# Optimization experiments

Hardware: AMD Instinct MI355X
Metric: run time of the kernel (lower is better)

The kernel has to match this reference:

```python
import jax, jax.numpy as jnp
import numpy as np

K_PRE = 500        # pre-NMS candidates per class (static-shape stand-in for boolean filter)
MAX_DET = 300      # max_detections_per_images
SCORE_THR = 0.05
NMS_THR = 0.5
MIN_SIZE = 0.01    # remove_small_boxes
BBOX_CLAMP = float(np.log(1000.0 / 16.0))


def setup_inputs():
    key = jax.random.key(0)
    k1, k2, k3, k4, k5, k6 = jax.random.split(key, 6)
    B, A, C = 2, 120000, 80
    H, W = 600, 960
    deltas = jax.random.normal(k1, (B, A, 4), jnp.float32) * 0.5
    scores = jax.random.uniform(k2, (B, A, C), jnp.float32)        # post-sigmoid class scores
    # realistic anchors: centers inside the image, sizes in [16, 256]
    cx = jax.random.uniform(k3, (B, A), jnp.float32) * W
    cy = jax.random.uniform(k4, (B, A), jnp.float32) * H
    aw = 16.0 + jax.random.uniform(k5, (B, A), jnp.float32) * 240.0
    ah = 16.0 + jax.random.uniform(k6, (B, A), jnp.float32) * 240.0
    anchors = jnp.stack([cx - aw / 2, cy - ah / 2, cx + aw / 2, cy + ah / 2], axis=-1)
    return {"deltas": deltas, "scores": scores, "anchors": anchors, "img_h": H, "img_w": W}


def _decode(deltas, anchors):
    # activ_2_bbox: standard dx,dy,dw,dh decode against xyxy anchors
    aw = anchors[..., 2] - anchors[..., 0]
    ah = anchors[..., 3] - anchors[..., 1]
    acx = anchors[..., 0] + 0.5 * aw
    acy = anchors[..., 1] + 0.5 * ah
    dx, dy = deltas[..., 0], deltas[..., 1]
    dw = jnp.minimum(deltas[..., 2], BBOX_CLAMP)
    dh = jnp.minimum(deltas[..., 3], BBOX_CLAMP)
    pcx = dx * aw + acx
    pcy = dy * ah + acy
    pw = jnp.exp(dw) * aw
    ph = jnp.exp(dh) * ah
    return jnp.stack([pcx - 0.5 * pw, pcy - 0.5 * ph, pcx + 0.5 * pw, pcy + 0.5 * ph], axis=-1)


def _iou(b):  # b: [K,4] -> [K,K]
    area = (b[:, 2] - b[:, 0]) * (b[:, 3] - b[:, 1])
    lt = jnp.maximum(b[:, None, :2], b[None, :, :2])
    rb = jnp.minimum(b[:, None, 2:], b[None, :, 2:])
    wh = jnp.maximum(rb - lt, 0.0)
    inter = wh[..., 0] * wh[..., 1]
    return inter / jnp.maximum(area[:, None] + area[None, :] - inter, 1e-9)


def _per_class(boxes, valid_size, scores_c):
    # boxes [A,4], valid_size [A] bool, scores_c [A]
    valid = valid_size & (scores_c > SCORE_THR)
    masked = jnp.where(valid, scores_c, -1.0)
    top_scores, idx = jax.lax.top_k(masked, K_PRE)      # sorted desc
    cboxes = boxes[idx]                                  # [K,4]
    cvalid = top_scores > SCORE_THR
    iou = _iou(cboxes)
    rng = jnp.arange(K_PRE)

    def body(i, keep):
        sup = keep[i] & (iou[i] > NMS_THR) & (rng > i)
        return keep & ~sup

    keep = jax.lax.stop_gradient(jax.lax.fori_loop(0, K_PRE, body, cvalid))
    # move kept detections to the front preserving score order, take first MAX_DET
    order = jnp.argsort(jnp.where(keep, rng, rng + K_PRE))[:MAX_DET]
    kb = cboxes[order]
    ks = top_scores[order]
    kv = keep[order]
    return jnp.concatenate(
        [jnp.where(kv[:, None], kb, 0.0), jnp.where(kv, ks, -1.0)[:, None]], axis=-1
    )  # [MAX_DET, 5] = (x1,y1,x2,y2,score); score=-1 marks padding


def _per_image(deltas_i, scores_i, anchors_i, img_h, img_w):
    boxes = _decode(deltas_i, anchors_i)  # [A,4]
    x1 = jnp.clip(boxes[..., 0], 0.0, float(img_w))
    y1 = jnp.clip(boxes[..., 1], 0.0, float(img_h))
    x2 = jnp.clip(boxes[..., 2], 0.0, float(img_w))
    y2 = jnp.clip(boxes[..., 3], 0.0, float(img_h))
    boxes = jnp.stack([x1, y1, x2, y2], axis=-1)
    valid_size = ((x2 - x1) >= MIN_SIZE) & ((y2 - y1) >= MIN_SIZE)
    return jax.vmap(_per_class, in_axes=(None, None, 1))(boxes, valid_size, scores_i)


def reference(deltas, scores, anchors, img_h, img_w):
    f = lambda d, s, a: _per_image(d, s, a, img_h, img_w)
    return jax.vmap(f)(deltas, scores, anchors)  # [B, C, MAX_DET, 5]
```

## Files before the change

### kernel.cpp

```cpp
#include <hip/hip_runtime.h>
#include <hip/hip_bf16.h>
#include <math.h>

#define BB 2
#define AA 120000
#define CC 80
#define K_PRE 500
#define MAX_DET 300
#define CAP 2048
#define NB2 256
#define SPEC_BIN 254
#define HB 1200
#define QPB 4000
#define APB 200
#define LBUF_G 512

#define OFF_BOXES   0
#define OFF_VALID   3840000
#define OFF_CNT     4161920
#define OFF_CAND    4163200

__global__ __launch_bounds__(256) void k_fused(
    const float* __restrict__ deltas, const float* __restrict__ anchors,
    const float* __restrict__ scores,
    const int* __restrict__ ih, const int* __restrict__ iw,
    float* __restrict__ boxes, unsigned char* __restrict__ valid,
    unsigned int* __restrict__ cnt, unsigned long long* __restrict__ cand)
{
    __shared__ unsigned char lvalid[APB];
    __shared__ unsigned long long lkey[LBUF_G];
    __shared__ unsigned short lcls[LBUF_G];
    __shared__ unsigned int lcnt[CC];
    __shared__ unsigned int lbase[CC];
    __shared__ unsigned int ltot;

    int blk   = blockIdx.x;
    int b     = blk / (HB / BB);
    int abase = blk * APB;
    int start = blk * QPB;
    int end   = start + QPB;

    if (threadIdx.x < CC) lcnt[threadIdx.x] = 0u;
    if (threadIdx.x == 0) ltot = 0u;

    if (threadIdx.x < APB) {
        int a = abase + threadIdx.x;
        float4 d  = ((const float4*)deltas)[a];
        float4 an = ((const float4*)anchors)[a];

        const float CLAMPF = (float)4.135166556742356;
        double W = (double)(*iw);
        double H = (double)(*ih);

        double aw  = (double)an.z - (double)an.x;
        double ah  = (double)an.w - (double)an.y;
        double acx = (double)an.x + 0.5 * aw;
        double acy = (double)an.y + 0.5 * ah;

        double dw = fmin((double)d.z, (double)CLAMPF);
        double dh = fmin((double)d.w, (double)CLAMPF);

        double pcx = (double)d.x * aw + acx;
        double pcy = (double)d.y * ah + acy;
        double pw  = exp(dw) * aw;
        double ph  = exp(dh) * ah;

        float x1 = (float)fmin(fmax(pcx - 0.5 * pw, 0.0), W);
        float y1 = (float)fmin(fmax(pcy - 0.5 * ph, 0.0), H);
        float x2 = (float)fmin(fmax(pcx + 0.5 * pw, 0.0), W);
        float y2 = (float)fmin(fmax(pcy + 0.5 * ph, 0.0), H);

        float4 bb; bb.x = x1; bb.y = y1; bb.z = x2; bb.w = y2;
        ((float4*)boxes)[a] = bb;
        unsigned char v = (((x2 - x1) >= 0.01f) && ((y2 - y1) >= 0.01f)) ? 1 : 0;
        valid[a] = v;
        lvalid[threadIdx.x] = v;
    }
    __syncthreads();

    const float4* s4 = (const float4*)scores;
    const float THRF = (float)SPEC_BIN;

    for (int i0 = start + threadIdx.x; i0 < end; i0 += 256 * 8) {
        int   ids[8];
        bool  has[8];
        float4 s[8];
        #pragma unroll
        for (int u = 0; u < 8; ++u) {
            int id = i0 + u * 256;
            has[u] = id < end;
            ids[u] = has[u] ? id : start;
        }
        #pragma unroll
        for (int u = 0; u < 8; ++u) s[u] = s4[ids[u]];
        #pragma unroll
        for (int u = 0; u < 8; ++u) {
            if (!has[u]) continue;
            float4 sv = s[u];
            float mx = fmaxf(fmaxf(sv.x, sv.y), fmaxf(sv.z, sv.w));
            if (mx * 256.0f >= THRF) {
                int rel = ids[u] - start;
                int la  = rel / 20;
                if (lvalid[la]) {
                    int q = rel % 20;
                    unsigned int ai = (unsigned int)(abase + la - b * AA);
                    unsigned long long lokey = (unsigned long long)(~ai);
                    float cv[4] = {sv.x, sv.y, sv.z, sv.w};
                    #pragma unroll
                    for (int cl = 0; cl < 4; ++cl) {
                        float sc = cv[cl];
                        if (sc * 256.0f >= THRF) {
                            int c = 4 * q + cl;
                            unsigned long long key =
                                (((unsigned long long)__float_as_uint(sc)) << 32) | lokey;
                            unsigned int p = atomicAdd(&ltot, 1u);
                            if (p < LBUF_G) {
                                lkey[p] = key;
                                lcls[p] = (unsigned short)c;
                                atomicAdd(&lcnt[c], 1u);
                            } else {
                                unsigned int pos = atomicAdd(&cnt[b * CC + c], 1u);
                                if (pos < CAP)
                                    cand[((size_t)(b * CC + c)) * CAP + pos] = key;
                            }
                        }
                    }
                }
            }
        }
    }
    __syncthreads();

    if (threadIdx.x < CC) {
        unsigned int nn = lcnt[threadIdx.x];
        if (nn) lbase[threadIdx.x] = atomicAdd(&cnt[b * CC + threadIdx.x], nn);
    }
    __syncthreads();

    unsigned int tot = min(ltot, (unsigned int)LBUF_G);
    for (unsigned int t = threadIdx.x; t < tot; t += 256) {
        int c = lcls[t];
        unsigned int pos = atomicAdd(&lbase[c], 1u);
        if (pos < CAP)
            cand[((size_t)(b * CC + c)) * CAP + pos] = lkey[t];
    }
}

__global__ __launch_bounds__(1024) void k_nms2(
    const float* __restrict__ boxes, const float* __restrict__ scores,
    const unsigned char* __restrict__ valid,
    const unsigned int* __restrict__ cnt, const unsigned long long* __restrict__ cand,
    float* __restrict__ out)
{
    __shared__ unsigned long long kb[2][2048];
    __shared__ unsigned int lh32[NB2];
    __shared__ int best;
    __shared__ unsigned int lpos;
    __shared__ float4 box4[512];
    __shared__ float  ar[512];
    __shared__ float  scs[512];
    __shared__ unsigned long long supT[512 * 9];
    __shared__ unsigned long long keepsh[8];
    __shared__ int pfx[9];

    int bc = blockIdx.x;
    int b  = bc / CC;
    int c  = bc % CC;
    int i  = threadIdx.x;
    const unsigned long long* cp = cand + (size_t)bc * CAP;

    int n = (int)cnt[bc];
    if (n < K_PRE || n > CAP) {
        unsigned long long* cpw = (unsigned long long*)cp;
        for (int t = i; t < NB2; t += 1024) lh32[t] = 0u;
        if (i == 0) { best = 0; lpos = 0u; }
        __syncthreads();
        for (int a = i; a < AA; a += 1024) {
            if (valid[b * AA + a]) {
                float sc = scores[((size_t)(b * AA + a)) * CC + c];
                if (sc > 0.05f) {
                    int bn = min((int)(sc * 256.0f), 255);
                    atomicAdd(&lh32[bn], 1u);
                }
            }
        }
        __syncthreads();
        if (i < NB2) {
            unsigned int s = 0;
            for (int j = i; j < NB2; ++j) s += lh32[j];
            if (s >= K_PRE) atomicMax(&best, i);
        }
        __syncthreads();
        int cut = best;
        for (int a = i; a < AA; a += 1024) {
            if (valid[b * AA + a]) {
                float sc = scores[((size_t)(b * AA + a)) * CC + c];
                if (sc > 0.05f) {
                    int bn = min((int)(sc * 256.0f), 255);
                    if (bn >= cut) {
                        unsigned int p = atomicAdd(&lpos, 1u);
                        if (p < CAP)
                            cpw[p] = (((unsigned long long)__float_as_uint(sc)) << 32)
                                     | (unsigned long long)(~(unsigned int)a);
                    }
                }
            }
        }
        __syncthreads();
        n = (int)min(lpos, (unsigned int)CAP);
    }

    unsigned long long key;

    if (n <= 1024) {
        key = (i < n) ? cp[i] : 0ull;
        int p = 0;
        for (unsigned int k = 2; k <= 1024; k <<= 1) {
            bool up = ((i & k) == 0);
            for (unsigned int j = k >> 1; j > 0; j >>= 1) {
                unsigned long long other;
                if (j >= 64) {
                    kb[p][i] = key;
                    __syncthreads();
                    other = kb[p][i ^ j];
                    p ^= 1;
                } else {
                    other = __shfl_xor(key, (int)j);
                }
                bool lower = ((i & j) == 0);
                bool keep_max = (lower == up);
                bool mine_big = key > other;
                key = (keep_max == mine_big) ? key : other;
            }
        }
    } else {
        unsigned long long kA = (i < n) ? cp[i] : 0ull;
        unsigned long long kB = (i + 1024 < n) ? cp[i + 1024] : 0ull;
        int tA = i, tB = i + 1024;
        int p = 0;
        for (unsigned int k = 2; k <= 2048; k <<= 1) {
            for (unsigned int j = k >> 1; j > 0; j >>= 1) {
                if (j == 1024) {
                    unsigned long long mx = (kA > kB) ? kA : kB;
                    unsigned long long mn = (kA > kB) ? kB : kA;
                    kA = mx; kB = mn;
                } else if (j >= 64) {
                    kb[p][tA] = kA; kb[p][tB] = kB;
                    __syncthreads();
                    unsigned long long oA = kb[p][tA ^ (int)j];
                    unsigned long long oB = kb[p][tB ^ (int)j];
                    p ^= 1;
                    { bool up = ((tA & k) == 0), lo = ((tA & j) == 0);
                      bool km = (lo == up), mb = kA > oA; kA = (km == mb) ? kA : oA; }
                    { bool up = ((tB & k) == 0), lo = ((tB & j) == 0);
                      bool km = (lo == up), mb = kB > oB; kB = (km == mb) ? kB : oB; }
                } else {
                    unsigned long long oA = __shfl_xor(kA, (int)j);
                    unsigned long long oB = __shfl_xor(kB, (int)j);
                    { bool up = ((tA & k) == 0), lo = ((tA & j) == 0);
                      bool km = (lo == up), mb = kA > oA; kA = (km == mb) ? kA : oA; }
                    { bool up = ((tB & k) == 0), lo = ((tB & j) == 0);
                      bool km = (lo == up), mb = kB > oB; kB = (km == mb) ? kB : oB; }
                }
            }
        }
        key = kA;
    }

    if (i < 512) {
        bool v = (key != 0ull);
        scs[i] = v ? __uint_as_float((unsigned int)(key >> 32)) : -1.0f;
        int a = v ? (int)(~(unsigned int)key) : 0;
        float4 bb = make_float4(0.f, 0.f, 0.f, 0.f);
        if (v && i < K_PRE) bb = ((const float4*)boxes)[(size_t)b * AA + a];
        box4[i] = bb;
        ar[i] = (bb.z - bb.x) * (bb.w - bb.y);
    }
    __syncthreads();

    int nv = min(n, K_PRE);

    {
        int wave = threadIdx.x >> 6;
        int lane = threadIdx.x & 63;
        for (int iw = 0; iw < 8; ++iw) {
            int ii = iw * 64 + lane;
            float4 bi = box4[ii];
            float ia = ar[ii];
            for (int j = iw * 64 + wave; j < nv; j += 16) {
                float4 bj = box4[j];
                float ja = ar[j];
                bool p = false;
                if (ii < j) {
                    float ltx = fmaxf(bi.x, bj.x);
                    float lty = fmaxf(bi.y, bj.y);
                    float rbx = fminf(bi.z, bj.z);
                    float rby = fminf(bi.w, bj.w);
                    float wx = fmaxf(rbx - ltx, 0.0f);
                    float wy = fmaxf(rby - lty, 0.0f);
                    float inter = wx * wy;
                    float den = fmaxf(ia + ja - inter, 1e-9f);
                    float h   = 0.5f * den;
                    float diff = inter - h;
                    if (fabsf(diff) > h * 9.5367431640625e-07f) {
                        p = diff > 0.0f;
                    } else {
                        p = (inter / den) > 0.5f;
                    }
                }
                unsigned long long m = __ballot(p);
                if (lane == 0) supT[j * 9 + iw] = m;
            }
        }
    }
    __syncthreads();

    if (threadIdx.x < 64) {
        int l = threadIdx.x;
        unsigned long long kept[8];
        #pragma unroll
        for (int w = 0; w < 8; ++w) {
            int j = w * 64 + l;
            bool vj = j < nv;
            bool ext = false;
            #pragma unroll
            for (int w2 = 0; w2 < 8; ++w2)
                if (w2 < w) ext = ext || (vj && (supT[j * 9 + w2] & kept[w2]) != 0ull);
            unsigned long long intra = vj ? supT[j * 9 + w] : 0ull;
            bool base = vj && !ext;
            unsigned long long kw = __ballot(base);
            for (int r = 0; r < 64; ++r) {
                bool k2 = base && ((intra & kw) == 0ull);
                unsigned long long nkw = __ballot(k2);
                if (nkw == kw) break;
                kw = nkw;
            }
            kept[w] = kw;
        }
        if (l < 8) keepsh[l] = kept[l];
    }
    __syncthreads();

    if (threadIdx.x == 0) {
        int s = 0;
        for (int w = 0; w < 8; ++w) { pfx[w] = s; s += __popcll(keepsh[w]); }
        pfx[8] = s;
    }
    __syncthreads();

    int total_kept = pfx[8];
    if (threadIdx.x < K_PRE) {
        int t = threadIdx.x;
        int w = t >> 6, bit = t & 63;
        unsigned long long kw = keepsh[w];
        bool kv = (kw >> bit) & 1ull;
        int kb2 = pfx[w] + __popcll(kw & ((bit == 0) ? 0ull : ((1ull << bit) - 1ull)));
        int p = kv ? kb2 : (total_kept + (t - kb2));
        if (p < MAX_DET) {
            float* o = out + ((size_t)bc * MAX_DET + p) * 5;
            if (kv) {
                float4 bb = box4[t];
                o[0] = bb.x; o[1] = bb.y; o[2] = bb.z; o[3] = bb.w; o[4] = scs[t];
            } else {
                o[0] = 0.f; o[1] = 0.f; o[2] = 0.f; o[3] = 0.f; o[4] = -1.0f;
            }
        }
    }
}

extern "C" void kernel_launch(void* const* d_in, const int* in_sizes, int n_in,
                              void* d_out, int out_size, void* d_ws, size_t ws_size,
                              hipStream_t stream)
{
    const float* deltas  = (const float*)d_in[0];
    const float* scores  = (const float*)d_in[1];
    const float* anchors = (const float*)d_in[2];
    const int*   ih      = (const int*)d_in[3];
    const int*   iw      = (const int*)d_in[4];
    float* out = (float*)d_out;

    char* w = (char*)d_ws;
    float*              boxes  = (float*)(w + OFF_BOXES);
    unsigned char*      valid  = (unsigned char*)(w + OFF_VALID);
    unsigned int*       cnt    = (unsigned int*)(w + OFF_CNT);
    unsigned long long* cand   = (unsigned long long*)(w + OFF_CAND);

    hipMemsetAsync(cnt, 0, BB * CC * sizeof(unsigned int), stream);
    k_fused<<<HB, 256, 0, stream>>>(deltas, anchors, scores, ih, iw,
                                    boxes, valid, cnt, cand);
    k_nms2<<<BB * CC, 1024, 0, stream>>>(boxes, scores, valid, cnt, cand, out);
}
```

Measured before the change: 175.6 us.

## Split sort and NMS stages into separate kernels with smaller LDS

Splits the fused sort+NMS kernel into two launches. k_sort does the top-K selection and writes sorted boxes, scores and the valid count back into the candidate workspace. k_mg then runs the IoU bitmask and greedy keep pass in 512-thread blocks with only the NMS shared memory. This lowers per-block LDS and thread count for the NMS stage, at the cost of an extra kernel launch and a global-memory round trip for the staged boxes.

```diff
diff --git a/kernel.cpp b/kernel.cpp
--- a/kernel.cpp
+++ b/kernel.cpp
@@ -146,32 +146,24 @@
     }
 }
 
-__global__ __launch_bounds__(1024) void k_nms2(
+__global__ __launch_bounds__(1024) void k_sort(
     const float* __restrict__ boxes, const float* __restrict__ scores,
     const unsigned char* __restrict__ valid,
-    const unsigned int* __restrict__ cnt, const unsigned long long* __restrict__ cand,
-    float* __restrict__ out)
+    const unsigned int* __restrict__ cnt, unsigned long long* __restrict__ cand)
 {
     __shared__ unsigned long long kb[2][2048];
     __shared__ unsigned int lh32[NB2];
     __shared__ int best;
     __shared__ unsigned int lpos;
-    __shared__ float4 box4[512];
-    __shared__ float  ar[512];
-    __shared__ float  scs[512];
-    __shared__ unsigned long long supT[512 * 9];
-    __shared__ unsigned long long keepsh[8];
-    __shared__ int pfx[9];
 
     int bc = blockIdx.x;
     int b  = bc / CC;
     int c  = bc % CC;
     int i  = threadIdx.x;
-    const unsigned long long* cp = cand + (size_t)bc * CAP;
+    unsigned long long* cp = cand + (size_t)bc * CAP;
 
     int n = (int)cnt[bc];
     if (n < K_PRE || n > CAP) {
-        unsigned long long* cpw = (unsigned long long*)cp;
         for (int t = i; t < NB2; t += 1024) lh32[t] = 0u;
         if (i == 0) { best = 0; lpos = 0u; }
         __syncthreads();
@@ -200,8 +192,8 @@
                     if (bn >= cut) {
                         unsigned int p = atomicAdd(&lpos, 1u);
                         if (p < CAP)
-                            cpw[p] = (((unsigned long long)__float_as_uint(sc)) << 32)
-                                     | (unsigned long long)(~(unsigned int)a);
+                            cp[p] = (((unsigned long long)__float_as_uint(sc)) << 32)
+                                    | (unsigned long long)(~(unsigned int)a);
                     }
                 }
             }
@@ -267,27 +259,50 @@
         key = kA;
     }
 
+    float4* sbox = (float4*)cp;
+    float*  ssc  = (float*)(cp + 1024);
+    int*    nvp  = (int*)(cp + 1280);
     if (i < 512) {
         bool v = (key != 0ull);
-        scs[i] = v ? __uint_as_float((unsigned int)(key >> 32)) : -1.0f;
+        float sc = v ? __uint_as_float((unsigned int)(key >> 32)) : -1.0f;
         int a = v ? (int)(~(unsigned int)key) : 0;
         float4 bb = make_float4(0.f, 0.f, 0.f, 0.f);
         if (v && i < K_PRE) bb = ((const float4*)boxes)[(size_t)b * AA + a];
-        box4[i] = bb;
-        ar[i] = (bb.z - bb.x) * (bb.w - bb.y);
-    }
-    __syncthreads();
-
-    int nv = min(n, K_PRE);
+        sbox[i] = bb;
+        ssc[i] = sc;
+    }
+    if (i == 0) nvp[0] = min(n, K_PRE);
+}
+
+__global__ __launch_bounds__(512) void k_mg(
+    const unsigned long long* __restrict__ cand, float* __restrict__ out)
+{
+    __shared__ float4 box4[512];
+    __shared__ float  ar[512];
+    __shared__ float  scs[512];
+    __shared__ unsigned long long supT[512 * 9];
+    __shared__ unsigned long long keepsh[8];
+    __shared__ int pfx[9];
+
+    int bc = blockIdx.x;
+    int tid = threadIdx.x;
+    const unsigned long long* cp = cand + (size_t)bc * CAP;
+
+    float4 bl = ((const float4*)cp)[tid];
+    box4[tid] = bl;
+    ar[tid]   = (bl.z - bl.x) * (bl.w - bl.y);
+    scs[tid]  = ((const float*)(cp + 1024))[tid];
+    int nv    = ((const int*)(cp + 1280))[0];
+    __syncthreads();
 
     {
-        int wave = threadIdx.x >> 6;
-        int lane = threadIdx.x & 63;
+        int wave = tid >> 6;
+        int lane = tid & 63;
         for (int iw = 0; iw < 8; ++iw) {
             int ii = iw * 64 + lane;
             float4 bi = box4[ii];
             float ia = ar[ii];
-            for (int j = iw * 64 + wave; j < nv; j += 16) {
+            for (int j = iw * 64 + wave; j < nv; j += 8) {
                 float4 bj = box4[j];
                 float ja = ar[j];
                 bool p = false;
@@ -315,13 +330,15 @@
     }
     __syncthreads();
 
-    if (threadIdx.x < 64) {
-        int l = threadIdx.x;
+    int nvv = nv;
+
+    if (tid < 64) {
+        int l = tid;
         unsigned long long kept[8];
         #pragma unroll
         for (int w = 0; w < 8; ++w) {
             int j = w * 64 + l;
-            bool vj = j < nv;
+            bool vj = j < nvv;
             bool ext = false;
             #pragma unroll
             for (int w2 = 0; w2 < 8; ++w2)
@@ -341,7 +358,7 @@
     }
     __syncthreads();
 
-    if (threadIdx.x == 0) {
+    if (tid == 0) {
         int s = 0;
         for (int w = 0; w < 8; ++w) { pfx[w] = s; s += __popcll(keepsh[w]); }
         pfx[8] = s;
@@ -349,8 +366,8 @@
     __syncthreads();
 
     int total_kept = pfx[8];
-    if (threadIdx.x < K_PRE) {
-        int t = threadIdx.x;
+    if (tid < K_PRE) {
+        int t = tid;
         int w = t >> 6, bit = t & 63;
         unsigned long long kw = keepsh[w];
         bool kv = (kw >> bit) & 1ull;
@@ -388,5 +405,6 @@
     hipMemsetAsync(cnt, 0, BB * CC * sizeof(unsigned int), stream);
     k_fused<<<HB, 256, 0, stream>>>(deltas, anchors, scores, ih, iw,
                                     boxes, valid, cnt, cand);
-    k_nms2<<<BB * CC, 1024, 0, stream>>>(boxes, scores, valid, cnt, cand, out);
+    k_sort<<<BB * CC, 1024, 0, stream>>>(boxes, scores, valid, cnt, cand);
+    k_mg<<<BB * CC, 512, 0, stream>>>(cand, out);
 }
```

After: 195.9 us. +11.6%, slower.

## Compute NMS suppression mask per thread over 64x64 tiles instead of ballots

Applied to the files above, without the earlier changes.

The pairwise IoU suppression matrix is now built from 36 upper-triangular 64x64 tiles. Each thread owns one box j and loops over the 64 boxes of a row block, accumulating the suppression bits in a register, so the per-pair __ballot and the single-lane LDS write are gone. This removes the wave-level sync per pair and the triangular waste from the old strided j loop. In exchange, the inner loop reads a broadcast LDS box for every k, and the work split is fixed at 36 chunks over 16 waves, which balances unevenly.

```diff
diff --git a/kernel.cpp b/kernel.cpp
--- a/kernel.cpp
+++ b/kernel.cpp
@@ -281,42 +281,59 @@
     int nv = min(n, K_PRE);
 
     {
-        int wave = threadIdx.x >> 6;
-        int lane = threadIdx.x & 63;
-        for (int iw = 0; iw < 8; ++iw) {
-            int ii = iw * 64 + lane;
-            float4 bi = box4[ii];
-            float ia = ar[ii];
-            for (int j = iw * 64 + wave; j < nv; j += 16) {
-                float4 bj = box4[j];
-                float ja = ar[j];
-                bool p = false;
-                if (ii < j) {
-                    float ltx = fmaxf(bi.x, bj.x);
-                    float lty = fmaxf(bi.y, bj.y);
-                    float rbx = fminf(bi.z, bj.z);
-                    float rby = fminf(bi.w, bj.w);
-                    float wx = fmaxf(rbx - ltx, 0.0f);
-                    float wy = fmaxf(rby - lty, 0.0f);
-                    float inter = wx * wy;
-                    float den = fmaxf(ia + ja - inter, 1e-9f);
-                    float h   = 0.5f * den;
-                    float diff = inter - h;
-                    if (fabsf(diff) > h * 9.5367431640625e-07f) {
-                        p = diff > 0.0f;
-                    } else {
-                        p = (inter / den) > 0.5f;
-                    }
-                }
-                unsigned long long m = __ballot(p);
-                if (lane == 0) supT[j * 9 + iw] = m;
-            }
-        }
-    }
-    __syncthreads();
-
-    if (threadIdx.x < 64) {
-        int l = threadIdx.x;
+        int wave = i >> 6;
+        int lane = i & 63;
+        for (int ci = wave; ci < 36; ci += 16) {
+            int iw;
+            if      (ci >= 35) iw = 7;
+            else if (ci >= 33) iw = 6;
+            else if (ci >= 30) iw = 5;
+            else if (ci >= 26) iw = 4;
+            else if (ci >= 21) iw = 3;
+            else if (ci >= 15) iw = 2;
+            else if (ci >=  8) iw = 1;
+            else               iw = 0;
+            int cst = (iw == 0) ? 0 : (iw == 1) ? 8 : (iw == 2) ? 15 :
+                      (iw == 3) ? 21 : (iw == 4) ? 26 : (iw == 5) ? 30 :
+                      (iw == 6) ? 33 : 35;
+            int co  = ci - cst;
+            int j   = (iw + co) * 64 + lane;
+            bool have = j < nv;
+            int js  = have ? j : 0;
+            float4 bj = box4[js];
+            float  ja = ar[js];
+            int base = iw * 64;
+            unsigned long long acc = 0ull;
+            #pragma unroll 16
+            for (int k = 0; k < 64; ++k) {
+                float4 bi = box4[base + k];
+                float  ia = ar[base + k];
+                float ltx = fmaxf(bi.x, bj.x);
+                float lty = fmaxf(bi.y, bj.y);
+                float rbx = fminf(bi.z, bj.z);
+                float rby = fminf(bi.w, bj.w);
+                float wx = fmaxf(rbx - ltx, 0.0f);
+                float wy = fmaxf(rby - lty, 0.0f);
+                float inter = wx * wy;
+                float den = fmaxf(ia + ja - inter, 1e-9f);
+                float h   = 0.5f * den;
+                float diff = inter - h;
+                bool p;
+                if (fabsf(diff) > h * 9.5367431640625e-07f) {
+                    p = diff > 0.0f;
+                } else {
+                    p = (inter / den) > 0.5f;
+                }
+                if (p) acc |= (1ull << k);
+            }
+            if (co == 0) acc &= (1ull << (j & 63)) - 1ull;
+            if (have) supT[j * 9 + iw] = acc;
+        }
+    }
+    __syncthreads();
+
+    if (i < 64) {
+        int l = i;
         unsigned long long kept[8];
         #pragma unroll
         for (int w = 0; w < 8; ++w) {
@@ -341,7 +358,7 @@
     }
     __syncthreads();
 
-    if (threadIdx.x == 0) {
+    if (i == 0) {
         int s = 0;
         for (int w = 0; w < 8; ++w) { pfx[w] = s; s += __popcll(keepsh[w]); }
         pfx[8] = s;
@@ -349,8 +366,8 @@
     __syncthreads();
 
     int total_kept = pfx[8];
-    if (threadIdx.x < K_PRE) {
-        int t = threadIdx.x;
+    if (i < K_PRE) {
+        int t = i;
         int w = t >> 6, bit = t & 63;
         unsigned long long kw = keepsh[w];
         bool kv = (kw >> bit) & 1ull;
```

Result: faster. 166.9 us (-4.9%).
